# Kernel tuning notes

Measured on AMD Instinct MI355X. Metric: run time of the kernel, lower is better.

The kernel has to match this reference:

```python
import jax, jax.numpy as jnp
import numpy as np

H, HKV, HD = 16, 16, 64  # num_heads, num_kv_heads, head_dim

def rotate_half(x):
    x1, x2 = jnp.split(x, 2, axis=-1)
    return jnp.concatenate((-x2, x1), axis=-1)

def setup_inputs() -> dict:
    key = jax.random.key(0)
    ks = jax.random.split(key, 4)
    B, L, D = 4, 2048, 1024
    hidden_states = jax.random.normal(ks[0], (B, L, D), jnp.float32)
    # RoPE tables [L, head_dim]
    inv_freq = 1.0 / (10000.0 ** (jnp.arange(0, HD, 2, dtype=jnp.float32) / HD))
    freqs = jnp.outer(jnp.arange(L, dtype=jnp.float32), inv_freq)
    emb = jnp.concatenate((freqs, freqs), axis=-1)
    cos, sin = jnp.cos(emb), jnp.sin(emb)
    active_mask = jax.random.randint(ks[1], (B, L), 0, 2).astype(bool)
    Wqkv = jax.random.normal(ks[2], ((H + 2 * HKV) * HD, D), jnp.float32) / np.sqrt(D)
    Wo = jax.random.normal(ks[3], (D, H * HD), jnp.float32) / np.sqrt(H * HD)
    return {"hidden_states": hidden_states, "cos": cos, "sin": sin,
            "active_mask": active_mask, "Wqkv": Wqkv, "Wo": Wo}

def reference(hidden_states, cos, sin, active_mask, Wqkv, Wo):
    B, L, D = hidden_states.shape
    qkv = (hidden_states @ Wqkv.T).reshape(B, L, H + 2 * HKV, HD)
    q = qkv[:, :, :H]
    k = qkv[:, :, H:H + HKV]
    v = qkv[:, :, H + HKV:]
    c = cos[:, None, :]  # [L,1,HD] broadcasts over B and heads
    s = sin[:, None, :]
    q = q * c + rotate_half(q) * s
    k = k * c + rotate_half(k) * s
    # sparse queries: only active positions emit queries
    q = q * active_mask[:, :, None, None].astype(q.dtype)
    scale = 1.0 / np.sqrt(HD)
    scores = jnp.einsum('bqhd,bkhd->bhqk', q, k) * scale  # [B,H,L,L]
    attn = jax.nn.softmax(scores, axis=-1)
    out = jnp.einsum('bhqk,bkhd->bqhd', attn, v).reshape(B, L, H * HD)
    out = out @ Wo.T
    return out * active_mask[:, :, None].astype(out.dtype)
```

## Files before the change

kernel.cpp:

```cpp
#include <hip/hip_runtime.h>
#include <cstdint>

typedef _Float16 f16;
typedef __attribute__((ext_vector_type(2))) __fp16 fp16v2;
typedef __attribute__((ext_vector_type(4))) _Float16 f16x4;
typedef __attribute__((ext_vector_type(8))) _Float16 f16x8;
typedef __attribute__((ext_vector_type(4))) float f32x4;
typedef __attribute__((ext_vector_type(16))) float f32x16;

#if __has_builtin(__builtin_amdgcn_exp2f)
#define EXP2F(x) __builtin_amdgcn_exp2f(x)
#else
#define EXP2F(x) exp2f(x)
#endif

#if __has_builtin(__builtin_amdgcn_fdot2)
#define FDOT2(a, b, c) __builtin_amdgcn_fdot2((a), (b), (c), false)
#else
#define FDOT2(a, b, c) ((c) + (float)(a)[0] * (float)(b)[0] + (float)(a)[1] * (float)(b)[1])
#endif

#define GLOAD_LDS16(gp, lp) \
  __builtin_amdgcn_global_load_lds((const __attribute__((address_space(1))) void*)(gp), \
                                   (__attribute__((address_space(3))) void*)(lp), 16, 0, 0)


__global__ __launch_bounds__(256) void cvt_all(const float4* __restrict__ h, f16x4* __restrict__ h16,
                                               const float4* __restrict__ wq, f16x4* __restrict__ wq16,
                                               const float4* __restrict__ wo, f16x4* __restrict__ wo16,
                                               const float* __restrict__ cosb, const float* __restrict__ sinb,
                                               float2* __restrict__ cst) {
  int i = blockIdx.x * 256 + threadIdx.x;
  if (i >= 3145728) {
    const int i2 = i - 3145728;
    const int d = i2 >> 11, l = i2 & 2047;
    cst[i2] = make_float2(cosb[l * 64 + d], sinb[l * 64 + d]);
    return;
  }
  const float4* src;
  f16x4* dst;
  if (i < 2097152) { src = h + i; dst = h16 + i; }
  else if (i < 2883584) { src = wq + (i - 2097152); dst = wq16 + (i - 2097152); }
  else { src = wo + (i - 2883584); dst = wo16 + (i - 2883584); }
  float4 v = *src;
  f16x4 o;
  o.x = (f16)v.x; o.y = (f16)v.y; o.z = (f16)v.z; o.w = (f16)v.w;
  *dst = o;
}

template<int EPI, int N, int K>
__global__ __launch_bounds__(256) void gemm_bt(
    const f16* __restrict__ A, const f16* __restrict__ Bm,
    f16* __restrict__ Qf, f16* __restrict__ Kf, f16* __restrict__ Vf,
    float* __restrict__ Cout, const int* __restrict__ mask,
    const float2* __restrict__ cst) {
  constexpr int NT = N / 128;
  const int bm = blockIdx.x / NT;
  const int bn = blockIdx.x % NT;
  const int lane = threadIdx.x & 63;
  const int wid  = threadIdx.x >> 6;
  const int wm = wid >> 1, wn = wid & 1;

  __shared__ f16 sA[128 * 32];
  __shared__ f16 sB[128 * 32];

  f32x4 acc[4][4] = {};

  const f16* Abase = A + (size_t)bm * 128 * K;
  const f16* Bbase = Bm + (size_t)bn * 128 * K;
  const int srow = lane >> 2;
  const int skk  = ((lane & 3) ^ ((lane >> 3) & 3)) * 8;

  const int lo = lane & 15;
  const int h16 = lane >> 4;
  const int xr = (lo >> 1) & 3;

#define GEMM_STAGE(k0)                                                        \
  do {                                                                        \
    __syncthreads();                                                          \
    _Pragma("unroll")                                                         \
    for (int c = 0; c < 2; ++c) {                                             \
      const int chunk = wid * 2 + c;                                          \
      GLOAD_LDS16(Abase + (chunk * 16 + srow) * K + (k0) + skk, &sA[chunk * 512]); \
      GLOAD_LDS16(Bbase + (chunk * 16 + srow) * K + (k0) + skk, &sB[chunk * 512]); \
    }                                                                         \
    __syncthreads();                                                          \
    _Pragma("unroll")                                                         \
    for (int i = 0; i < 4; ++i) {                                             \
      af[i] = *(const f16x8*)&sA[(wm * 64 + i * 16 + lo) * 32 + (h16 ^ xr) * 8]; \
      bf[i] = *(const f16x8*)&sB[(wn * 64 + i * 16 + lo) * 32 + (h16 ^ xr) * 8]; \
    }                                                                         \
  } while (0)

  const bool swp = (EPI == 1) && (bn < 16);
  if (swp) {
    for (int k0 = 0; k0 < K; k0 += 32) {
      f16x8 af[4], bf[4];
      GEMM_STAGE(k0);
      #pragma unroll
      for (int i = 0; i < 4; ++i)
        #pragma unroll
        for (int j = 0; j < 4; ++j)
          acc[i][j] = __builtin_amdgcn_mfma_f32_16x16x32_f16(bf[i], af[j], acc[i][j], 0, 0, 0);
    }
  } else {
    for (int k0 = 0; k0 < K; k0 += 32) {
      f16x8 af[4], bf[4];
      GEMM_STAGE(k0);
      #pragma unroll
      for (int i = 0; i < 4; ++i)
        #pragma unroll
        for (int j = 0; j < 4; ++j)
          acc[i][j] = __builtin_amdgcn_mfma_f32_16x16x32_f16(af[i], bf[j], acc[i][j], 0, 0, 0);
    }
  }

  if constexpr (EPI == 1) {
    const int head = bn * 2 + wn;
    if (head < 32) {
      f16* dst = (head < 16) ? Qf : Kf;
      const int h15 = head & 15;
      const int bb = bm >> 4;
      const int llbase = (bm & 15) * 128 + wm * 64;
      const int ahi = h16 >> 1, kkl = h16 & 1;
      f16* base = dst + (size_t)(bb * 16 + h15) * 64 * 2048;
      #pragma unroll
      for (int j = 0; j < 4; ++j) {
        const int ll = llbase + j * 16 + lo;
        float msc = 1.0f;
        if (head < 16) msc = mask[bb * 2048 + ll] ? 0.18033688011112042f : 0.0f;
        union { f16x8 v; fp16v2 hh[4]; } u0, u1;
        #pragma unroll
        for (int i = 0; i < 2; ++i) {
          float y0[4], y1[4];
          #pragma unroll
          for (int r = 0; r < 4; ++r) {
            const float2 cs = cst[(size_t)(i * 16 + 4 * h16 + r) * 2048 + ll];
            const float xl = acc[i][j][r], xh = acc[i + 2][j][r];
            y0[r] = (xl * cs.x - xh * cs.y) * msc;
            y1[r] = (xh * cs.x + xl * cs.y) * msc;
          }
          u0.hh[i * 2 + 0] = __builtin_amdgcn_cvt_pkrtz(y0[0], y0[1]);
          u0.hh[i * 2 + 1] = __builtin_amdgcn_cvt_pkrtz(y0[2], y0[3]);
          u1.hh[i * 2 + 0] = __builtin_amdgcn_cvt_pkrtz(y1[0], y1[1]);
          u1.hh[i * 2 + 1] = __builtin_amdgcn_cvt_pkrtz(y1[2], y1[3]);
        }
        const int t = ll >> 5, q5 = ll & 31;
        f16* p = base + (size_t)t * 2048 + (ahi * 32 + q5) * 8;
        *(f16x8*)(p + (kkl + 0) * 512) = u0.v;
        *(f16x8*)(p + (kkl + 2) * 512) = u1.v;
      }
    } else {
      const int hv = head - 32;
      #pragma unroll
      for (int i = 0; i < 4; ++i) {
        #pragma unroll
        for (int j = 0; j < 4; ++j) {
          #pragma unroll
          for (int r = 0; r < 4; ++r) {
            const int gm = bm * 128 + wm * 64 + i * 16 + (lane >> 4) * 4 + r;
            const int bb = gm >> 11, ll = gm & 2047;
            const int dd = j * 16 + lo;
            const int k = ll & 31;
            const int i32 = (k & ~12) | ((k & 4) << 1) | ((k & 8) >> 1);
            const int cc = i32 >> 4, hih = (i32 >> 3) & 1, jj = i32 & 7;
            const int blk = dd >> 5, qq = dd & 31;
            Vf[((size_t)(bb * 16 + hv) * 64 + (ll >> 5)) * 2048 +
               (cc * 2 + blk) * 512 + hih * 256 + qq * 8 + jj] = (f16)acc[i][j][r];
          }
        }
      }
    }
  } else {
    #pragma unroll
    for (int i = 0; i < 4; ++i) {
      #pragma unroll
      for (int j = 0; j < 4; ++j) {
        #pragma unroll
        for (int r = 0; r < 4; ++r) {
          const int gm = bm * 128 + wm * 64 + i * 16 + (lane >> 4) * 4 + r;
          const int gn = bn * 128 + wn * 64 + j * 16 + lo;
          const float mv = mask[gm] ? 1.0f : 0.0f;
          Cout[(size_t)gm * 1024 + gn] = acc[i][j][r] * mv;
        }
      }
    }
  }
#undef GEMM_STAGE
}

#define LOADKV(kd, vd, kp, vp)                       \
  do {                                               \
    _Pragma("unroll")                                \
    for (int _i = 0; _i < 4; ++_i) {                 \
      kd[_i] = *(const f16x8*)&(kp)[_i * 512];       \
      vd[_i] = *(const f16x8*)&(vp)[_i * 512];       \
    }                                                \
  } while (0)

#define ATTN_BODY(kr, vr)                                                        \
  do {                                                                           \
    f32x16 s = {};                                                               \
    __builtin_amdgcn_s_setprio(1);                                               \
    _Pragma("unroll")                                                            \
    for (int _k = 0; _k < 4; ++_k)                                               \
      s = __builtin_amdgcn_mfma_f32_32x32x16_f16(kr[_k], qf[_k], s, 0, 0, 0);    \
    __builtin_amdgcn_s_setprio(0);                                               \
    union PU { fp16v2 h[4]; f16x8 v; } pb0, pb1;                                 \
    _Pragma("unroll")                                                            \
    for (int _i = 0; _i < 4; ++_i) {                                             \
      pb0.h[_i] = __builtin_amdgcn_cvt_pkrtz(EXP2F(s[2 * _i]), EXP2F(s[2 * _i + 1]));       \
      pb1.h[_i] = __builtin_amdgcn_cvt_pkrtz(EXP2F(s[8 + 2 * _i]), EXP2F(s[8 + 2 * _i + 1])); \
      la = FDOT2(pb0.h[_i], kOne, la);                                           \
      lb = FDOT2(pb1.h[_i], kOne, lb);                                           \
    }                                                                            \
    __builtin_amdgcn_s_setprio(1);                                               \
    o0 = __builtin_amdgcn_mfma_f32_32x32x16_f16(vr[0], pb0.v, o0, 0, 0, 0);      \
    o1 = __builtin_amdgcn_mfma_f32_32x32x16_f16(vr[1], pb0.v, o1, 0, 0, 0);      \
    o0 = __builtin_amdgcn_mfma_f32_32x32x16_f16(vr[2], pb1.v, o0, 0, 0, 0);      \
    o1 = __builtin_amdgcn_mfma_f32_32x32x16_f16(vr[3], pb1.v, o1, 0, 0, 0);      \
    __builtin_amdgcn_s_setprio(0);                                               \
  } while (0)

__global__ __launch_bounds__(512) void attn_kernel(const f16* __restrict__ Qf,
                                                   const f16* __restrict__ Kf,
                                                   const f16* __restrict__ Vf,
                                                   f16* __restrict__ Ow) {
  const int bid = (blockIdx.x & 7) * 128 + (blockIdx.x >> 3);
  const int bh = bid >> 4;
  const int qt = bid & 15;
  const int lane = threadIdx.x & 63;
  const int wid = threadIdx.x >> 6;
  const int qw = wid & 3;
  const int kvh = wid >> 2;
  const int hi = lane >> 5;
  const int q = lane & 31;
  const int qr = qt * 128 + qw * 32 + q;

  __shared__ float o_lds[4][32][65];
  __shared__ float l_lds[4][32];

  const f16* Qb = Qf + (size_t)bh * 64 * 2048;
  const f16* Kb = Kf + (size_t)bh * 64 * 2048;
  const f16* Vb = Vf + (size_t)bh * 64 * 2048;

  f16x8 qf[4];
  {
    const f16* qtb = Qb + (size_t)(qt * 4 + qw) * 2048 + lane * 8;
    #pragma unroll
    for (int kk = 0; kk < 4; ++kk)
      qf[kk] = *(const f16x8*)&qtb[kk * 512];
  }

  f32x16 o0 = {}, o1 = {};
  float la = 0.0f, lb = 0.0f;
  const fp16v2 kOne = {(__fp16)1.0f, (__fp16)1.0f};

  const f16* kptr = Kb + (size_t)(kvh * 32) * 2048 + lane * 8;
  const f16* vptr = Vb + (size_t)(kvh * 32) * 2048 + lane * 8;
  f16x8 ka[4], va[4], kn[4], vn[4];
  LOADKV(ka, va, kptr, vptr);
  for (int t = 0; t < 32; t += 2) {
    LOADKV(kn, vn, kptr + 2048, vptr + 2048);
    ATTN_BODY(ka, va);
    if (t + 2 < 32)
      LOADKV(ka, va, kptr + 4096, vptr + 4096);
    ATTN_BODY(kn, vn);
    kptr += 4096; vptr += 4096;
  }

  float lhalf = la + lb;
  lhalf += __shfl_xor(lhalf, 32, 64);

  if (kvh == 1) {
    #pragma unroll
    for (int blk = 0; blk < 2; ++blk)
      #pragma unroll
      for (int g = 0; g < 4; ++g)
        #pragma unroll
        for (int j = 0; j < 4; ++j)
          o_lds[qw][q][blk * 32 + g * 8 + 4 * hi + j] = blk ? o1[g * 4 + j] : o0[g * 4 + j];
    if (hi == 0) l_lds[qw][q] = lhalf;
  }
  __syncthreads();
  if (kvh == 0) {
    const float inv = 1.0f / (lhalf + l_lds[qw][q]);
    const int b = bh >> 4, h = bh & 15;
    f16* orow = Ow + ((size_t)(b * 2048 + qr)) * 1024 + h * 64;
    #pragma unroll
    for (int blk = 0; blk < 2; ++blk) {
      #pragma unroll
      for (int g = 0; g < 4; ++g) {
        f16x4 st;
        #pragma unroll
        for (int j = 0; j < 4; ++j) {
          const int d = blk * 32 + g * 8 + 4 * hi + j;
          const float v = ((blk ? o1[g * 4 + j] : o0[g * 4 + j]) + o_lds[qw][q][d]) * inv;
          st[j] = (f16)v;
        }
        *(f16x4*)&orow[blk * 32 + g * 8 + 4 * hi] = st;
      }
    }
  }
}

extern "C" void kernel_launch(void* const* d_in, const int* in_sizes, int n_in,
                              void* d_out, int out_size, void* d_ws, size_t ws_size,
                              hipStream_t stream) {
  const float* hidden = (const float*)d_in[0];
  const float* cosb   = (const float*)d_in[1];
  const float* sinb   = (const float*)d_in[2];
  const int*   mask   = (const int*)d_in[3];
  const float* wqkv   = (const float*)d_in[4];
  const float* wo     = (const float*)d_in[5];
  float* out = (float*)d_out;
  char* ws = (char*)d_ws;

  f16* h16    = (f16*)(ws + 0);
  f16* wqkv16 = (f16*)(ws + 16777216);
  f16* wo16   = (f16*)(ws + 23068672);
  f16* Qfb    = (f16*)(ws + 25165824);
  f16* Kfb    = (f16*)(ws + 41943040);
  f16* Vfb    = (f16*)(ws + 58720256);
  float2* cst = (float2*)(ws + 75497472);
  f16* Ow     = h16;

  cvt_all<<<12544, 256, 0, stream>>>((const float4*)hidden, (f16x4*)h16,
                                     (const float4*)wqkv, (f16x4*)wqkv16,
                                     (const float4*)wo, (f16x4*)wo16,
                                     cosb, sinb, cst);

  gemm_bt<1, 3072, 1024><<<64 * 24, 256, 0, stream>>>(h16, wqkv16, Qfb, Kfb, Vfb,
                                                      nullptr, mask, cst);

  attn_kernel<<<1024, 512, 0, stream>>>(Qfb, Kfb, Vfb, Ow);

  gemm_bt<2, 1024, 1024><<<64 * 8, 256, 0, stream>>>(Ow, wo16, nullptr, nullptr, nullptr,
                                                     out, mask, nullptr);
}
```

Before: 200.2 us.

## Process two 32-row query tiles per wave to reuse loaded K/V fragments

```diff
diff --git a/kernel.cpp b/kernel.cpp
--- a/kernel.cpp
+++ b/kernel.cpp
@@ -198,27 +198,41 @@
     }                                                \
   } while (0)
 
-#define ATTN_BODY(kr, vr)                                                        \
+#define ATTN_BODY64(kr, vr)                                                      \
   do {                                                                           \
-    f32x16 s = {};                                                               \
+    f32x16 sa = {}, sb = {};                                                     \
     __builtin_amdgcn_s_setprio(1);                                               \
     _Pragma("unroll")                                                            \
     for (int _k = 0; _k < 4; ++_k)                                               \
-      s = __builtin_amdgcn_mfma_f32_32x32x16_f16(kr[_k], qf[_k], s, 0, 0, 0);    \
+      sa = __builtin_amdgcn_mfma_f32_32x32x16_f16(kr[_k], qfa[_k], sa, 0, 0, 0); \
+    _Pragma("unroll")                                                            \
+    for (int _k = 0; _k < 4; ++_k)                                               \
+      sb = __builtin_amdgcn_mfma_f32_32x32x16_f16(kr[_k], qfb[_k], sb, 0, 0, 0); \
     __builtin_amdgcn_s_setprio(0);                                               \
-    union PU { fp16v2 h[4]; f16x8 v; } pb0, pb1;                                 \
+    union PU { fp16v2 h[4]; f16x8 v; } pa0, pa1, pb0, pb1;                       \
     _Pragma("unroll")                                                            \
     for (int _i = 0; _i < 4; ++_i) {                                             \
-      pb0.h[_i] = __builtin_amdgcn_cvt_pkrtz(EXP2F(s[2 * _i]), EXP2F(s[2 * _i + 1]));       \
-      pb1.h[_i] = __builtin_amdgcn_cvt_pkrtz(EXP2F(s[8 + 2 * _i]), EXP2F(s[8 + 2 * _i + 1])); \
-      la = FDOT2(pb0.h[_i], kOne, la);                                           \
+      pa0.h[_i] = __builtin_amdgcn_cvt_pkrtz(EXP2F(sa[2 * _i]), EXP2F(sa[2 * _i + 1]));       \
+      pa1.h[_i] = __builtin_amdgcn_cvt_pkrtz(EXP2F(sa[8 + 2 * _i]), EXP2F(sa[8 + 2 * _i + 1])); \
+      la = FDOT2(pa0.h[_i], kOne, la);                                           \
+      la = FDOT2(pa1.h[_i], kOne, la);                                           \
+    }                                                                            \
+    _Pragma("unroll")                                                            \
+    for (int _i = 0; _i < 4; ++_i) {                                             \
+      pb0.h[_i] = __builtin_amdgcn_cvt_pkrtz(EXP2F(sb[2 * _i]), EXP2F(sb[2 * _i + 1]));       \
+      pb1.h[_i] = __builtin_amdgcn_cvt_pkrtz(EXP2F(sb[8 + 2 * _i]), EXP2F(sb[8 + 2 * _i + 1])); \
+      lb = FDOT2(pb0.h[_i], kOne, lb);                                           \
       lb = FDOT2(pb1.h[_i], kOne, lb);                                           \
     }                                                                            \
     __builtin_amdgcn_s_setprio(1);                                               \
-    o0 = __builtin_amdgcn_mfma_f32_32x32x16_f16(vr[0], pb0.v, o0, 0, 0, 0);      \
-    o1 = __builtin_amdgcn_mfma_f32_32x32x16_f16(vr[1], pb0.v, o1, 0, 0, 0);      \
-    o0 = __builtin_amdgcn_mfma_f32_32x32x16_f16(vr[2], pb1.v, o0, 0, 0, 0);      \
-    o1 = __builtin_amdgcn_mfma_f32_32x32x16_f16(vr[3], pb1.v, o1, 0, 0, 0);      \
+    oa0 = __builtin_amdgcn_mfma_f32_32x32x16_f16(vr[0], pa0.v, oa0, 0, 0, 0);    \
+    oa1 = __builtin_amdgcn_mfma_f32_32x32x16_f16(vr[1], pa0.v, oa1, 0, 0, 0);    \
+    ob0 = __builtin_amdgcn_mfma_f32_32x32x16_f16(vr[0], pb0.v, ob0, 0, 0, 0);    \
+    ob1 = __builtin_amdgcn_mfma_f32_32x32x16_f16(vr[1], pb0.v, ob1, 0, 0, 0);    \
+    oa0 = __builtin_amdgcn_mfma_f32_32x32x16_f16(vr[2], pa1.v, oa0, 0, 0, 0);    \
+    oa1 = __builtin_amdgcn_mfma_f32_32x32x16_f16(vr[3], pa1.v, oa1, 0, 0, 0);    \
+    ob0 = __builtin_amdgcn_mfma_f32_32x32x16_f16(vr[2], pb1.v, ob0, 0, 0, 0);    \
+    ob1 = __builtin_amdgcn_mfma_f32_32x32x16_f16(vr[3], pb1.v, ob1, 0, 0, 0);    \
     __builtin_amdgcn_s_setprio(0);                                               \
   } while (0)
 
@@ -226,33 +240,36 @@
                                                    const f16* __restrict__ Kf,
                                                    const f16* __restrict__ Vf,
                                                    f16* __restrict__ Ow) {
-  const int bid = (blockIdx.x & 7) * 128 + (blockIdx.x >> 3);
-  const int bh = bid >> 4;
-  const int qt = bid & 15;
+  const int bid = (blockIdx.x & 7) * 64 + (blockIdx.x >> 3);
+  const int bh = bid >> 3;
+  const int qt = bid & 7;
   const int lane = threadIdx.x & 63;
   const int wid = threadIdx.x >> 6;
   const int qw = wid & 3;
   const int kvh = wid >> 2;
   const int hi = lane >> 5;
   const int q = lane & 31;
-  const int qr = qt * 128 + qw * 32 + q;
-
-  __shared__ float o_lds[4][32][65];
-  __shared__ float l_lds[4][32];
+
+  __shared__ float o_lds[8][32][65];
+  __shared__ float l_lds[8][32];
 
   const f16* Qb = Qf + (size_t)bh * 64 * 2048;
   const f16* Kb = Kf + (size_t)bh * 64 * 2048;
   const f16* Vb = Vf + (size_t)bh * 64 * 2048;
 
-  f16x8 qf[4];
+  const int ta = qt * 8 + qw * 2;
+  f16x8 qfa[4], qfb[4];
   {
-    const f16* qtb = Qb + (size_t)(qt * 4 + qw) * 2048 + lane * 8;
+    const f16* pa = Qb + (size_t)ta * 2048 + lane * 8;
+    const f16* pb = pa + 2048;
     #pragma unroll
-    for (int kk = 0; kk < 4; ++kk)
-      qf[kk] = *(const f16x8*)&qtb[kk * 512];
-  }
-
-  f32x16 o0 = {}, o1 = {};
+    for (int kk = 0; kk < 4; ++kk) {
+      qfa[kk] = *(const f16x8*)&pa[kk * 512];
+      qfb[kk] = *(const f16x8*)&pb[kk * 512];
+    }
+  }
+
+  f32x16 oa0 = {}, oa1 = {}, ob0 = {}, ob1 = {};
   float la = 0.0f, lb = 0.0f;
   const fp16v2 kOne = {(__fp16)1.0f, (__fp16)1.0f};
 
@@ -262,15 +279,15 @@
   LOADKV(ka, va, kptr, vptr);
   for (int t = 0; t < 32; t += 2) {
     LOADKV(kn, vn, kptr + 2048, vptr + 2048);
-    ATTN_BODY(ka, va);
+    ATTN_BODY64(ka, va);
     if (t + 2 < 32)
       LOADKV(ka, va, kptr + 4096, vptr + 4096);
-    ATTN_BODY(kn, vn);
+    ATTN_BODY64(kn, vn);
     kptr += 4096; vptr += 4096;
   }
 
-  float lhalf = la + lb;
-  lhalf += __shfl_xor(lhalf, 32, 64);
+  float lha = la + __shfl_xor(la, 32, 64);
+  float lhb = lb + __shfl_xor(lb, 32, 64);
 
   if (kvh == 1) {
     #pragma unroll
@@ -278,27 +295,34 @@
       #pragma unroll
       for (int g = 0; g < 4; ++g)
         #pragma unroll
-        for (int j = 0; j < 4; ++j)
-          o_lds[qw][q][blk * 32 + g * 8 + 4 * hi + j] = blk ? o1[g * 4 + j] : o0[g * 4 + j];
-    if (hi == 0) l_lds[qw][q] = lhalf;
+        for (int j = 0; j < 4; ++j) {
+          const int d = blk * 32 + g * 8 + 4 * hi + j;
+          o_lds[qw * 2 + 0][q][d] = blk ? oa1[g * 4 + j] : oa0[g * 4 + j];
+          o_lds[qw * 2 + 1][q][d] = blk ? ob1[g * 4 + j] : ob0[g * 4 + j];
+        }
+    if (hi == 0) { l_lds[qw * 2 + 0][q] = lha; l_lds[qw * 2 + 1][q] = lhb; }
   }
   __syncthreads();
   if (kvh == 0) {
-    const float inv = 1.0f / (lhalf + l_lds[qw][q]);
+    const float inva = 1.0f / (lha + l_lds[qw * 2 + 0][q]);
+    const float invb = 1.0f / (lhb + l_lds[qw * 2 + 1][q]);
     const int b = bh >> 4, h = bh & 15;
-    f16* orow = Ow + ((size_t)(b * 2048 + qr)) * 1024 + h * 64;
+    const int qra = qt * 256 + qw * 64 + q;
+    f16* orowa = Ow + ((size_t)(b * 2048 + qra)) * 1024 + h * 64;
+    f16* orowb = orowa + 32 * 1024;
     #pragma unroll
     for (int blk = 0; blk < 2; ++blk) {
       #pragma unroll
       for (int g = 0; g < 4; ++g) {
-        f16x4 st;
+        f16x4 sta, stb;
         #pragma unroll
         for (int j = 0; j < 4; ++j) {
           const int d = blk * 32 + g * 8 + 4 * hi + j;
-          const float v = ((blk ? o1[g * 4 + j] : o0[g * 4 + j]) + o_lds[qw][q][d]) * inv;
-          st[j] = (f16)v;
-        }
-        *(f16x4*)&orow[blk * 32 + g * 8 + 4 * hi] = st;
+          sta[j] = (f16)(((blk ? oa1[g * 4 + j] : oa0[g * 4 + j]) + o_lds[qw * 2 + 0][q][d]) * inva);
+          stb[j] = (f16)(((blk ? ob1[g * 4 + j] : ob0[g * 4 + j]) + o_lds[qw * 2 + 1][q][d]) * invb);
+        }
+        *(f16x4*)&orowa[blk * 32 + g * 8 + 4 * hi] = sta;
+        *(f16x4*)&orowb[blk * 32 + g * 8 + 4 * hi] = stb;
       }
     }
   }
@@ -333,7 +357,7 @@
   gemm_bt<1, 3072, 1024><<<64 * 24, 256, 0, stream>>>(h16, wqkv16, Qfb, Kfb, Vfb,
                                                       nullptr, mask, cst);
 
-  attn_kernel<<<1024, 512, 0, stream>>>(Qfb, Kfb, Vfb, Ow);
+  attn_kernel<<<512, 512, 0, stream>>>(Qfb, Kfb, Vfb, Ow);
 
   gemm_bt<2, 1024, 1024><<<64 * 8, 256, 0, stream>>>(Ow, wo16, nullptr, nullptr, nullptr,
                                                      out, mask, nullptr);
```

New measurement: 188.4 us. -5.9%, faster.
